# Performance work log

Measured on AMD Instinct MI355X. Metric: run time of the kernel, lower is better.

## Reference

```python
import jax, jax.numpy as jnp
import numpy as np

B, N, D, K = 16, 1024, 512, 8
NUM_ITERS = 3
EPS = 1e-08
LN_EPS = 1e-05


def layer_norm(x, g, b):
    m = jnp.mean(x, axis=-1, keepdims=True)
    v = jnp.var(x, axis=-1, keepdims=True)
    return (x - m) * jax.lax.rsqrt(v + LN_EPS) * g + b


def setup_inputs() -> dict:
    key = jax.random.key(0)
    ks = jax.random.split(key, 8)
    s = 1.0 / np.sqrt(D)
    return {
        "embeddings": jax.random.normal(ks[0], (B, N, D), jnp.float32),
        "noise_init": jax.random.normal(ks[1], (B, K, D), jnp.float32),
        "noise_final": jax.random.normal(ks[2], (B, K, D), jnp.float32),
        "slots_mu": jax.random.normal(ks[3], (1, K, D), jnp.float32) * s,
        "slots_logsigma": jax.random.normal(ks[4], (1, K, D), jnp.float32) * s,
        "mixing_coeffs": jnp.ones((1, K), jnp.float32) / K,
        "Wk": jax.random.normal(ks[5], (D, D), jnp.float32) * s,
        "bk": jnp.zeros((D,), jnp.float32),
        "Wq": jax.random.normal(ks[6], (D, D), jnp.float32) * s,
        "bq": jnp.zeros((D,), jnp.float32),
        "Wv": jax.random.normal(ks[7], (D, D), jnp.float32) * s,
        "bv": jnp.zeros((D,), jnp.float32),
        "ln_g": jnp.ones((D,), jnp.float32),
        "ln_b": jnp.zeros((D,), jnp.float32),
    }


def reference(embeddings, noise_init, noise_final, slots_mu, slots_logsigma,
              mixing_coeffs, Wk, bk, Wq, bq, Wv, bv, ln_g, ln_b):
    b, n, d = embeddings.shape
    mixing = jnp.broadcast_to(mixing_coeffs, (b, K))           # [B,K]
    mu = jnp.broadcast_to(slots_mu, (b, K, d))                 # [B,K,D]
    sigma = jnp.exp(jnp.broadcast_to(slots_logsigma, (b, K, d)))
    slots = mu + sigma * noise_init                            # sampled slots

    x = layer_norm(embeddings, ln_g, ln_b)
    keys = x @ Wk + bk                                         # [B,N,D]
    values = x @ Wv + bv                                       # [B,N,D]
    # slots are never updated inside the loop, so queries are loop-invariant
    queries = slots @ Wq + bq                                  # [B,K,D]

    log2pi = jnp.float32(np.log(2.0 * np.pi))
    attn = None
    for _ in range(NUM_ITERS):
        diff = keys[:, :, None, :] - queries[:, None, :, :]    # [B,N,K,D]
        gll = -0.5 * jnp.sum(diff * diff / (sigma[:, None] ** 2 + EPS), axis=-1)  # [B,N,K]
        gll = (-0.5 * d * log2pi
               - 0.5 * jnp.sum(jnp.log(jnp.abs(sigma) + EPS), axis=-1)[:, None, :]
               + gll)
        attn = mixing[:, None, :] * gll                        # [B,N,K]
        attn = attn / jnp.sum(attn, axis=-1, keepdims=True)
        attn = attn / (jnp.sum(attn, axis=1, keepdims=True) + EPS)
        mu = jnp.einsum('bnk,bnd->bkd', attn, values)          # [B,K,D]
        diff2 = values[:, :, None, :] - mu[:, None, :, :]      # [B,N,K,D]
        sigma = jnp.einsum('bnk,bnkd->bkd', attn, diff2 * diff2)
        mixing = jnp.sum(attn, axis=1) / n

    sigma = jnp.maximum(jnp.abs(sigma), EPS)
    slots = mu + sigma * noise_final
    return slots, jnp.transpose(attn, (0, 2, 1))
```

## Files before the change

### kernel.cpp

```cpp
#include <hip/hip_runtime.h>
#include <math.h>

#define BB 16
#define NN 1024
#define DD 512
#define KK 8
#define EPS_ 1e-8f
#define LN_EPS_ 1e-5f
#define GLL_C0 (-470.4965290007924f)

typedef __attribute__((ext_vector_type(8))) short short8;
typedef __attribute__((ext_vector_type(4))) short short4v;
typedef __attribute__((ext_vector_type(4))) float f32x4;

static __device__ inline short f2bf(float f) {
    unsigned u = __builtin_bit_cast(unsigned, f);
    u = (u + 0x7fff + ((u >> 16) & 1)) >> 16;
    return (short)u;
}
static __device__ inline float bf2f(short s) {
    unsigned u = ((unsigned)(unsigned short)s) << 16;
    return __builtin_bit_cast(float, u);
}
static __device__ inline void gload16(const void* g, void* l) {
    __builtin_amdgcn_global_load_lds(
        (const __attribute__((address_space(1))) void*)g,
        (__attribute__((address_space(3))) void*)l, 16, 0, 0);
}

struct Params {
    const float *emb, *noise_init, *noise_final, *slots_mu, *slots_logsg,
                *mixing_co, *Wk, *bk, *Wq, *bq, *Wv, *bv, *ln_g, *ln_b;
    float *out;
    float *queries, *attn, *s1p, *s2p, *off, *mix16, *colsum;
    short *Abf, *E, *Vbf, *WtKV, *WqT, *slotbf, *F_bt;
};

__global__ __launch_bounds__(256) void k_pre(Params p)
{
    __shared__ __align__(16) short eb[4352];
    int u = blockIdx.x, tid = threadIdx.x;
    if (u < 4096) {
        int row  = u * 4 + (tid >> 6);
        int lane = tid & 63;
        const float* e = p.emb + (size_t)row * DD + lane * 8;
        float4 v0 = *(const float4*)e;
        float4 v1 = *(const float4*)(e + 4);
        float v[8] = {v0.x, v0.y, v0.z, v0.w, v1.x, v1.y, v1.z, v1.w};
        float s = 0.0f;
#pragma unroll
        for (int j = 0; j < 8; j++) s += v[j];
#pragma unroll
        for (int off = 32; off; off >>= 1) s += __shfl_xor(s, off);
        float m = s * (1.0f / DD);
        float vs = 0.0f;
#pragma unroll
        for (int j = 0; j < 8; j++) { float d = v[j] - m; vs = fmaf(d, d, vs); }
#pragma unroll
        for (int off = 32; off; off >>= 1) vs += __shfl_xor(vs, off);
        float rstd = rsqrtf(vs * (1.0f / DD) + LN_EPS_);

        float4 g0 = *(const float4*)&p.ln_g[lane * 8];
        float4 g1 = *(const float4*)&p.ln_g[lane * 8 + 4];
        float4 b0 = *(const float4*)&p.ln_b[lane * 8];
        float4 b1 = *(const float4*)&p.ln_b[lane * 8 + 4];
        float g[8] = {g0.x, g0.y, g0.z, g0.w, g1.x, g1.y, g1.z, g1.w};
        float bb[8] = {b0.x, b0.y, b0.z, b0.w, b1.x, b1.y, b1.z, b1.w};
        short8 o;
#pragma unroll
        for (int j = 0; j < 8; j++) o[j] = f2bf(fmaf((v[j] - m) * rstd, g[j], bb[j]));
        *(short8*)&p.Abf[(size_t)row * DD + lane * 8] = o;
    } else if (u < 4864) {
        int idx = u - 4096;
        int z = idx >> 8, rem = idx & 255;
        const float* W = (z == 0) ? p.Wk : (z == 1) ? p.Wv : p.Wq;
        short* T; int nbase;
        if (z < 2) { T = p.WtKV; nbase = z * 512; } else { T = p.WqT; nbase = 0; }
        int k0 = (rem & 15) * 32, n0 = (rem >> 4) * 32;
        int tx = tid & 31, ty = tid >> 5;
        float (*t)[33] = (float (*)[33])eb;
#pragma unroll
        for (int q = 0; q < 4; q++)
            t[ty + q * 8][tx] = W[(size_t)(k0 + ty + q * 8) * DD + n0 + tx];
        __syncthreads();
#pragma unroll
        for (int q = 0; q < 4; q++)
            T[(size_t)(nbase + n0 + ty + q * 8) * DD + k0 + tx] = f2bf(t[tx][ty + q * 8]);
    } else {
        int idx = u - 4864;
        int b = idx >> 3, k = idx & 7;
#pragma unroll
        for (int q = 0; q < 2; q++) {
            int d = tid + q * 256;
            float sg = expf(p.slots_logsg[k * DD + d]);
            float sl = fmaf(sg, p.noise_init[((size_t)(b * KK + k)) * DD + d],
                            p.slots_mu[k * DD + d]);
            p.slotbf[((size_t)(b * KK + k)) * DD + d] = f2bf(sl);
        }
    }
}

__global__ __launch_bounds__(256) void k_gemm(Params p)
{
    __shared__ __align__(16) short smem[32768];
    int u = blockIdx.x, tid = threadIdx.x;
    int w = tid >> 6, l = tid & 63;
    int x = u & 7, by = u >> 3;
    int qmode = (by == 128);
    if (qmode && x >= 4) return;
    const short* A  = qmode ? p.slotbf : p.Abf + (size_t)by * 128 * DD;
    const short* Bt = qmode ? p.WqT : p.WtKV;
    int row0 = qmode ? 0 : by * 128;
    int col0 = x * 128;

    int sr = l >> 3;
    int sg_off = ((l & 7) ^ sr) * 8;
    int mq = (w & 1) * 64, nq = (w >> 1) * 64;
    int fr = l & 15;
    int orow = (l >> 4) * 4, ocol = l & 15;

#define STAGE(buf, k0)                                                        \
    {                                                                         \
        short* As_ = smem + (buf) * 8192;                                     \
        short* Bs_ = smem + 16384 + (buf) * 8192;                             \
        _Pragma("unroll")                                                     \
        for (int j = 0; j < 4; j++) {                                         \
            int rb = w * 32 + j * 8;                                          \
            int r  = rb + sr;                                                 \
            gload16(A  + (size_t)r * DD + (k0) + sg_off, &As_[rb * 64 + l * 8]);   \
            gload16(Bt + (size_t)(col0 + r) * DD + (k0) + sg_off, &Bs_[rb * 64 + l * 8]); \
        }                                                                     \
    }

    f32x4 acc[4][4] = {};
    STAGE(0, 0);
    __syncthreads();
    for (int i = 0; i < 8; i++) {
        if (i < 7) STAGE((i + 1) & 1, (i + 1) * 64);
        const short* As_ = smem + (i & 1) * 8192;
        const short* Bs_ = smem + 16384 + (i & 1) * 8192;
#pragma unroll
        for (int kk = 0; kk < 2; kk++) {
            int g = kk * 4 + (l >> 4);
            short8 af[4], bfv[4];
#pragma unroll
            for (int mi = 0; mi < 4; mi++)
                af[mi] = *(const short8*)&As_[(mq + mi * 16 + fr) * 64 + (g ^ (fr & 7)) * 8];
#pragma unroll
            for (int ni = 0; ni < 4; ni++)
                bfv[ni] = *(const short8*)&Bs_[(nq + ni * 16 + fr) * 64 + (g ^ (fr & 7)) * 8];
#pragma unroll
            for (int mi = 0; mi < 4; mi++)
#pragma unroll
                for (int ni = 0; ni < 4; ni++)
                    acc[mi][ni] = __builtin_amdgcn_mfma_f32_16x16x32_bf16(
                        af[mi], bfv[ni], acc[mi][ni], 0, 0, 0);
        }
        __syncthreads();
    }
#undef STAGE

    float bvv[4];
#pragma unroll
    for (int ni = 0; ni < 4; ni++) {
        int col = col0 + nq + ni * 16 + ocol;
        bvv[ni] = qmode ? p.bq[col] : (x < 4 ? p.bk[col] : p.bv[col - 512]);
    }

    if (qmode) {
#pragma unroll
        for (int ni = 0; ni < 4; ni++) {
            int col = col0 + nq + ni * 16 + ocol;
#pragma unroll
            for (int mi = 0; mi < 4; mi++)
#pragma unroll
                for (int r = 0; r < 4; r++)
                    p.queries[(size_t)(mq + mi * 16 + orow + r) * DD + col] =
                        acc[mi][ni][r] + bvv[ni];
        }
    } else {
        short* eb = smem;
        int npass = (x < 4) ? 2 : 1;
        for (int pass = 0; pass < npass; pass++) {
#pragma unroll
            for (int mi = 0; mi < 4; mi++)
#pragma unroll
                for (int r = 0; r < 4; r++) {
                    int row = mq + mi * 16 + orow + r;
                    int sw = ((row >> 2) & 3) << 1;
#pragma unroll
                    for (int ni = 0; ni < 4; ni++) {
                        int colg = nq + ni * 16 + ocol;
                        float val = acc[mi][ni][r] + bvv[ni];
                        if (x < 4 && pass == 0) val = val * val;
                        eb[row * 128 + (((colg >> 3) ^ sw) * 8) + (colg & 7)] = f2bf(val);
                    }
                }
            __syncthreads();
#pragma unroll
            for (int i = 0; i < 8; i++) {
                int row = i * 16 + w * 4 + (l >> 4);
                int c = l & 15;
                int cc = c ^ (((row >> 2) & 3) << 1);
                short8 vv = *(const short8*)&eb[row * 128 + cc * 8];
                if (x < 4) {
                    size_t a = (size_t)(row0 + row) * 1024 +
                               (pass ? 512 + col0 : col0) + c * 8;
                    *(short8*)&p.E[a] = vv;
                } else {
                    *(short8*)&p.Vbf[(size_t)(row0 + row) * 512 +
                                     (col0 - 512) + c * 8] = vv;
                }
            }
            __syncthreads();
        }
    }
}

__global__ __launch_bounds__(256) void k_fprep0(Params p)
{
    __shared__ float red[512];
    int u = blockIdx.x, tid = threadIdx.x;
    int b = u >> 4, k = u & 15;
    short* Fr = p.F_bt + (size_t)(b * 16 + k) * 1024;
    if (k >= KK) {
        short4v zv = {0, 0, 0, 0};
        *(short4v*)&Fr[tid * 4] = zv;
        if (tid == 0) { p.off[b * 16 + k] = 0.0f; p.mix16[b * 16 + k] = 0.0f; }
        return;
    }
    float* rc = red;
    float* rl = red + 256;
    float c = 0.0f, ld = 0.0f;
#pragma unroll
    for (int q = 0; q < 2; q++) {
        int d = tid * 2 + q;
        float sg = expf(p.slots_logsg[k * DD + d]);
        float iv = 1.0f / (sg * sg + EPS_);
        float qv = p.queries[((size_t)(b * KK + k)) * DD + d];
        Fr[d]       = f2bf(-0.5f * iv);
        Fr[512 + d] = f2bf(qv * iv);
        c  = fmaf(qv * qv, iv, c);
        ld += logf(fabsf(sg) + EPS_);
    }
    rc[tid] = c; rl[tid] = ld;
    __syncthreads();
    for (int s = 128; s > 0; s >>= 1) {
        if (tid < s) { rc[tid] += rc[tid + s]; rl[tid] += rl[tid + s]; }
        __syncthreads();
    }
    if (tid == 0) {
        p.off[b * 16 + k]    = GLL_C0 - 0.5f * rl[0] - 0.5f * rc[0];
        p.mix16[b * 16 + k]  = p.mixing_co[k];
        p.colsum[b * KK + k] = 0.0f;
    }
}

__global__ __launch_bounds__(256) void k_gllmu(Params p)
{
    __shared__ f32x4 red[2][64];
    __shared__ float asml[32 * KK];
    int u = blockIdx.x, tid = threadIdx.x;
    int w = tid >> 6, l = tid & 63;
    int b = u >> 5, chunk = u & 31;
    int n0 = chunk * 32;
    int t = w & 1, khalf = w >> 1;

    const short* Ea = p.E + ((size_t)(b * NN + n0 + t * 16 + (l & 15))) * 1024
                      + khalf * 512 + (l >> 4) * 8;
    const short* Fa = p.F_bt + (size_t)(b * 16 + (l & 15)) * 1024
                      + khalf * 512 + (l >> 4) * 8;
    f32x4 acc0 = {}, acc1 = {};
#pragma unroll
    for (int j = 0; j < 8; j++) {
        short8 a0 = *(const short8*)&Ea[j * 64];
        short8 f0 = *(const short8*)&Fa[j * 64];
        acc0 = __builtin_amdgcn_mfma_f32_16x16x32_bf16(a0, f0, acc0, 0, 0, 0);
        short8 a1 = *(const short8*)&Ea[j * 64 + 32];
        short8 f1 = *(const short8*)&Fa[j * 64 + 32];
        acc1 = __builtin_amdgcn_mfma_f32_16x16x32_bf16(a1, f1, acc1, 0, 0, 0);
    }
    f32x4 acc = acc0 + acc1;

    if (khalf) red[t][l] = acc;
    __syncthreads();
    if (!khalf) {
        acc += red[t][l];
        int col = l & 15;
        int rloc = t * 16 + (l >> 4) * 4;
        float offv = p.off[b * 16 + col];
        float mixv = p.mix16[b * 16 + col];
        float a[4], den[4];
#pragma unroll
        for (int r = 0; r < 4; r++) {
            a[r] = mixv * (acc[r] + offv);
            den[r] = a[r];
        }
#pragma unroll
        for (int mask = 1; mask <= 8; mask <<= 1)
#pragma unroll
            for (int r = 0; r < 4; r++) den[r] += __shfl_xor(den[r], mask);
        float csl = 0.0f;
        if (col < KK) {
#pragma unroll
            for (int r = 0; r < 4; r++) {
                float vv = a[r] / den[r];
                asml[(rloc + r) * KK + col] = vv;
                p.attn[((size_t)(b * NN + n0 + rloc + r)) * KK + col] = vv;
                csl += vv;
            }
        }
        csl += __shfl_xor(csl, 16);
        csl += __shfl_xor(csl, 32);
        if (l < KK) atomicAdd(&p.colsum[b * KK + l], csl);
    }
    __syncthreads();

    int d0 = tid * 2;
    float s1[2][KK] = {}, s2[2][KK] = {};
    const short* vb = p.Vbf + ((size_t)(b * NN + n0)) * DD + d0;
#pragma unroll 4
    for (int nn = 0; nn < 32; nn++) {
        short2 vs = *(const short2*)&vb[(size_t)nn * DD];
        float v0 = bf2f(vs.x), v1 = bf2f(vs.y);
        float v0q = v0 * v0, v1q = v1 * v1;
        float4 a0 = *(const float4*)&asml[nn * KK];
        float4 a1 = *(const float4*)&asml[nn * KK + 4];
        float aa[8] = {a0.x, a0.y, a0.z, a0.w, a1.x, a1.y, a1.z, a1.w};
#pragma unroll
        for (int k = 0; k < KK; k++) {
            s1[0][k] = fmaf(aa[k], v0, s1[0][k]);
            s2[0][k] = fmaf(aa[k], v0q, s2[0][k]);
            s1[1][k] = fmaf(aa[k], v1, s1[1][k]);
            s2[1][k] = fmaf(aa[k], v1q, s2[1][k]);
        }
    }
    size_t base = ((size_t)(b * 32 + chunk) * KK) * DD + d0;
#pragma unroll
    for (int k = 0; k < KK; k++) {
        *(float2*)&p.s1p[base + (size_t)k * DD] = make_float2(s1[0][k], s1[1][k]);
        *(float2*)&p.s2p[base + (size_t)k * DD] = make_float2(s2[0][k], s2[1][k]);
    }
}

__global__ __launch_bounds__(256) void k_fprep(Params p)
{
    __shared__ float red[512];
    int u = blockIdx.x, tid = threadIdx.x;
    int b = u >> 3, k = u & 7;
    float cs   = p.colsum[b * KK + k];
    float inv  = 1.0f / (cs + EPS_);
    float ssum = cs * inv;
    short* Fr = p.F_bt + (size_t)(b * 16 + k) * 1024;
    float* rc = red;
    float* rl = red + 256;
    float c = 0.0f, ld = 0.0f;
#pragma unroll
    for (int q = 0; q < 2; q++) {
        int d = tid * 2 + q;
        float s1 = 0.0f, s2 = 0.0f;
#pragma unroll
        for (int ns = 0; ns < 32; ns++) {
            size_t o = ((size_t)(b * 32 + ns) * KK + k) * DD + d;
            s1 += p.s1p[o];
            s2 += p.s2p[o];
        }
        float m  = s1 * inv;
        float sg = s2 * inv - m * m * (2.0f - ssum);
        float iv = 1.0f / (sg * sg + EPS_);
        float qv = p.queries[((size_t)(b * KK + k)) * DD + d];
        Fr[d]       = f2bf(-0.5f * iv);
        Fr[512 + d] = f2bf(qv * iv);
        c  = fmaf(qv * qv, iv, c);
        ld += logf(fabsf(sg) + EPS_);
    }
    rc[tid] = c; rl[tid] = ld;
    __syncthreads();
    for (int s = 128; s > 0; s >>= 1) {
        if (tid < s) { rc[tid] += rc[tid + s]; rl[tid] += rl[tid + s]; }
        __syncthreads();
    }
    if (tid == 0) {
        p.off[b * 16 + k]    = GLL_C0 - 0.5f * rl[0] - 0.5f * rc[0];
        p.mix16[b * 16 + k]  = ssum * (1.0f / NN);
        p.colsum[b * KK + k] = 0.0f;
    }
}

__global__ __launch_bounds__(256) void k_final(Params p)
{
    int u = blockIdx.x, tid = threadIdx.x;
    if (u < 256) {
        int gid = u * 256 + tid;
        int d = gid & 511;
        int k = (gid >> 9) & 7;
        int b = gid >> 12;
        float s1 = 0.0f, s2 = 0.0f;
#pragma unroll
        for (int ns = 0; ns < 32; ns++) {
            size_t o = ((size_t)(b * 32 + ns) * KK + k) * DD + d;
            s1 += p.s1p[o];
            s2 += p.s2p[o];
        }
        float cs   = p.colsum[b * KK + k];
        float inv  = 1.0f / (cs + EPS_);
        float ssum = cs * inv;
        float m    = s1 * inv;
        float sg   = s2 * inv - m * m * (2.0f - ssum);
        p.out[gid] = fmaf(fmaxf(fabsf(sg), EPS_), p.noise_final[gid], m);
    } else {
        int gid = (u - 256) * 256 + tid;
        int b = gid >> 13;
        int k = (gid >> 10) & 7;
        int n = gid & 1023;
        float cs = p.colsum[b * KK + k];
        p.out[BB * KK * DD + gid] =
            p.attn[((size_t)(b * NN + n)) * KK + k] / (cs + EPS_);
    }
}

extern "C" void kernel_launch(void* const* d_in, const int* in_sizes, int n_in,
                              void* d_out, int out_size, void* d_ws, size_t ws_size,
                              hipStream_t stream)
{
    Params pp;
    pp.emb         = (const float*)d_in[0];
    pp.noise_init  = (const float*)d_in[1];
    pp.noise_final = (const float*)d_in[2];
    pp.slots_mu    = (const float*)d_in[3];
    pp.slots_logsg = (const float*)d_in[4];
    pp.mixing_co   = (const float*)d_in[5];
    pp.Wk          = (const float*)d_in[6];
    pp.bk          = (const float*)d_in[7];
    pp.Wq          = (const float*)d_in[8];
    pp.bq          = (const float*)d_in[9];
    pp.Wv          = (const float*)d_in[10];
    pp.bv          = (const float*)d_in[11];
    pp.ln_g        = (const float*)d_in[12];
    pp.ln_b        = (const float*)d_in[13];
    pp.out         = (float*)d_out;

    float* ws = (float*)d_ws;
    pp.queries = ws;
    pp.attn    = pp.queries + BB * KK * DD;
    pp.s1p     = pp.attn + BB * NN * KK;
    pp.s2p     = pp.s1p + (size_t)BB * 32 * KK * DD;
    pp.off     = pp.s2p + (size_t)BB * 32 * KK * DD;
    pp.mix16   = pp.off + BB * 16;
    pp.colsum  = pp.mix16 + BB * 16;
    pp.Abf     = (short*)(pp.colsum + BB * KK);
    pp.E       = pp.Abf + (size_t)BB * NN * DD;
    pp.Vbf     = pp.E + (size_t)BB * NN * 1024;
    pp.WtKV    = pp.Vbf + (size_t)BB * NN * DD;
    pp.WqT     = pp.WtKV + (size_t)1024 * DD;
    pp.slotbf  = pp.WqT + (size_t)DD * DD;
    pp.F_bt    = pp.slotbf + (size_t)BB * KK * DD;

    k_pre<<<4992, 256, 0, stream>>>(pp);
    k_gemm<<<1032, 256, 0, stream>>>(pp);
    k_fprep0<<<256, 256, 0, stream>>>(pp);
    for (int it = 0; it < 3; it++) {
        k_gllmu<<<512, 256, 0, stream>>>(pp);
        if (it < 2) k_fprep<<<128, 256, 0, stream>>>(pp);
    }
    k_final<<<768, 256, 0, stream>>>(pp);
}
```

Measured before the change: 219.1 us.

## Stage GEMM tiles through registers with single LDS buffer and remap block order

Replaces the double-buffered direct global-to-LDS loads in the K/V/Q projection GEMM with register prefetch: the next tile is loaded into registers while MFMAs run on the current LDS tile, then written to a single LDS buffer after a barrier. This halves LDS use, which may allow more resident blocks, but adds a second barrier per iteration and extra VGPRs. It also changes the block-index mapping so consecutive blocks share the same weight column tile rather than the same row tile, which changes L2 reuse.

```diff
diff --git a/kernel.cpp b/kernel.cpp
--- a/kernel.cpp
+++ b/kernel.cpp
@@ -12,6 +12,7 @@
 typedef __attribute__((ext_vector_type(8))) short short8;
 typedef __attribute__((ext_vector_type(4))) short short4v;
 typedef __attribute__((ext_vector_type(4))) float f32x4;
+typedef __attribute__((ext_vector_type(4))) int int4v;
 
 static __device__ inline short f2bf(float f) {
     unsigned u = __builtin_bit_cast(unsigned, f);
@@ -21,11 +22,6 @@
 static __device__ inline float bf2f(short s) {
     unsigned u = ((unsigned)(unsigned short)s) << 16;
     return __builtin_bit_cast(float, u);
-}
-static __device__ inline void gload16(const void* g, void* l) {
-    __builtin_amdgcn_global_load_lds(
-        (const __attribute__((address_space(1))) void*)g,
-        (__attribute__((address_space(3))) void*)l, 16, 0, 0);
 }
 
 struct Params {
@@ -102,53 +98,60 @@
 
 __global__ __launch_bounds__(256) void k_gemm(Params p)
 {
-    __shared__ __align__(16) short smem[32768];
+    __shared__ __align__(16) short smem[16384];
     int u = blockIdx.x, tid = threadIdx.x;
     int w = tid >> 6, l = tid & 63;
-    int x = u & 7, by = u >> 3;
-    int qmode = (by == 128);
-    if (qmode && x >= 4) return;
+    int x, by, qmode;
+    if (u >= 1024) { qmode = 1; x = u - 1024; if (x >= 4) return; by = 128; }
+    else           { qmode = 0; x = u >> 7;   by = u & 127; }
     const short* A  = qmode ? p.slotbf : p.Abf + (size_t)by * 128 * DD;
     const short* Bt = qmode ? p.WqT : p.WtKV;
     int row0 = qmode ? 0 : by * 128;
     int col0 = x * 128;
 
+    short* As = smem;
+    short* Bs = smem + 8192;
     int sr = l >> 3;
     int sg_off = ((l & 7) ^ sr) * 8;
     int mq = (w & 1) * 64, nq = (w >> 1) * 64;
     int fr = l & 15;
     int orow = (l >> 4) * 4, ocol = l & 15;
 
-#define STAGE(buf, k0)                                                        \
-    {                                                                         \
-        short* As_ = smem + (buf) * 8192;                                     \
-        short* Bs_ = smem + 16384 + (buf) * 8192;                             \
-        _Pragma("unroll")                                                     \
-        for (int j = 0; j < 4; j++) {                                         \
-            int rb = w * 32 + j * 8;                                          \
-            int r  = rb + sr;                                                 \
-            gload16(A  + (size_t)r * DD + (k0) + sg_off, &As_[rb * 64 + l * 8]);   \
-            gload16(Bt + (size_t)(col0 + r) * DD + (k0) + sg_off, &Bs_[rb * 64 + l * 8]); \
-        }                                                                     \
-    }
+    int4v ra[4], rb4[4];
+    auto LOADR = [&](int k0) {
+#pragma unroll
+        for (int j = 0; j < 4; j++) {
+            int rbj = w * 32 + j * 8;
+            int r   = rbj + sr;
+            ra[j]  = *(const int4v*)(A  + (size_t)r * DD + k0 + sg_off);
+            rb4[j] = *(const int4v*)(Bt + (size_t)(col0 + r) * DD + k0 + sg_off);
+        }
+    };
+    auto WRITES = [&]() {
+#pragma unroll
+        for (int j = 0; j < 4; j++) {
+            int rbj = w * 32 + j * 8;
+            *(int4v*)&As[rbj * 64 + l * 8] = ra[j];
+            *(int4v*)&Bs[rbj * 64 + l * 8] = rb4[j];
+        }
+    };
 
     f32x4 acc[4][4] = {};
-    STAGE(0, 0);
+    LOADR(0);
+    WRITES();
     __syncthreads();
     for (int i = 0; i < 8; i++) {
-        if (i < 7) STAGE((i + 1) & 1, (i + 1) * 64);
-        const short* As_ = smem + (i & 1) * 8192;
-        const short* Bs_ = smem + 16384 + (i & 1) * 8192;
+        if (i < 7) LOADR((i + 1) * 64);
 #pragma unroll
         for (int kk = 0; kk < 2; kk++) {
             int g = kk * 4 + (l >> 4);
             short8 af[4], bfv[4];
 #pragma unroll
             for (int mi = 0; mi < 4; mi++)
-                af[mi] = *(const short8*)&As_[(mq + mi * 16 + fr) * 64 + (g ^ (fr & 7)) * 8];
+                af[mi] = *(const short8*)&As[(mq + mi * 16 + fr) * 64 + (g ^ (fr & 7)) * 8];
 #pragma unroll
             for (int ni = 0; ni < 4; ni++)
-                bfv[ni] = *(const short8*)&Bs_[(nq + ni * 16 + fr) * 64 + (g ^ (fr & 7)) * 8];
+                bfv[ni] = *(const short8*)&Bs[(nq + ni * 16 + fr) * 64 + (g ^ (fr & 7)) * 8];
 #pragma unroll
             for (int mi = 0; mi < 4; mi++)
 #pragma unroll
@@ -157,8 +160,11 @@
                         af[mi], bfv[ni], acc[mi][ni], 0, 0, 0);
         }
         __syncthreads();
-    }
-#undef STAGE
+        if (i < 7) {
+            WRITES();
+            __syncthreads();
+        }
+    }
 
     float bvv[4];
 #pragma unroll
```

Result: slower. 229.8 us (+4.9%).
